# Kernel optimization log

Hardware: AMD Instinct MI355X
Metric: run time of the kernel (lower is better)

The kernel has to match this reference:

```python
import jax, jax.numpy as jnp
import numpy as np

L, N, E, H = 1024, 8, 1024, 8


def setup_inputs() -> dict:
    key = jax.random.key(0)
    ks = jax.random.split(key, 9)
    s = 0.02
    return {
        "query": jax.random.normal(ks[0], (L, N, E), jnp.float32),
        "key": jax.random.normal(ks[1], (L, N, E), jnp.float32),
        "value": jax.random.normal(ks[2], (L, N, E), jnp.float32),
        "Wqkv": jax.random.normal(ks[3], (H, 3 * E, E), jnp.float32) * s,
        "bqkv": jax.random.normal(ks[4], (H, 3 * E), jnp.float32) * s,
        "Wo": jax.random.normal(ks[5], (H, E, E), jnp.float32) * s,
        "bo": jax.random.normal(ks[6], (H, E), jnp.float32) * s,
        "Wout": jax.random.normal(ks[7], (E, H * E), jnp.float32) * s,
        "bout": jax.random.normal(ks[8], (E,), jnp.float32) * s,
    }


def reference(query, key, value, Wqkv, bqkv, Wo, bo, Wout, bout):
    # Each of H independent single-head MultiheadAttention modules, batched over h.
    Wq, Wk, Wv = Wqkv[:, :E], Wqkv[:, E:2 * E], Wqkv[:, 2 * E:]   # [H,E,E] each
    bq, bk, bv = bqkv[:, :E], bqkv[:, E:2 * E], bqkv[:, 2 * E:]   # [H,E]
    # Projections: (L,N,E) x (H,E,E) -> (H,L,N,E)
    q = jnp.einsum('lne,hde->hlnd', query, Wq) + bq[:, None, None, :]
    k = jnp.einsum('sne,hde->hsnd', key, Wk) + bk[:, None, None, :]
    v = jnp.einsum('sne,hde->hsnd', value, Wv) + bv[:, None, None, :]
    scale = 1.0 / jnp.sqrt(jnp.asarray(E, q.dtype))  # head_dim == E since 1 head per module
    scores = jnp.einsum('hlnd,hsnd->hnls', q, k) * scale  # [H,N,L,S]
    attn_weights = jax.nn.softmax(scores, axis=-1)
    ctx = jnp.einsum('hnls,hsnd->hlnd', attn_weights, v)   # [H,L,N,E]
    head_out = jnp.einsum('hlnd,hed->hlne', ctx, Wo) + bo[:, None, None, :]
    # concat along last dim: (L,N,H*E)
    concat = jnp.transpose(head_out, (1, 2, 0, 3)).reshape(L, N, H * E)
    out = concat @ Wout.T + bout  # (L,N,E)
    return out, attn_weights  # weights: [H,N,L,S] (stack of per-head (N,L,S))
```

## Files before the change

kernel.cpp:

```cpp
#include <hip/hip_runtime.h>
#include <stdint.h>


typedef unsigned short u16;
typedef unsigned int u32;
typedef __attribute__((ext_vector_type(8))) __bf16 bf16x8;
typedef __attribute__((ext_vector_type(4))) float f32x4;
typedef __attribute__((ext_vector_type(4))) u16 u16x4;

#define DEVFN static __device__ __forceinline__

static constexpr int LQ = 1024, NN = 8, EE = 1024, HH = 8, SS = 1024;
static constexpr long LNE = (long)LQ * NN * EE;
static constexpr long MM = 1048576;

static constexpr long OF_QBF   = 0;
static constexpr long OF_KBF   = 8388608;
static constexpr long OF_VALT  = 16777216;
static constexpr long OF_F     = 25165824;
static constexpr long OF_WKT   = 33554432;
static constexpr long OF_WVT   = 41943040;
static constexpr long OF_WOT   = 50331648;
static constexpr long OF_WOUTB = 58720256;
static constexpr long OF_GT    = 67108864;
static constexpr long OF_BM    = 75497472;
static constexpr long OF_T     = 83886080;
static constexpr long OF_P     = 150994944;
static constexpr long OF_SMALL_F = 109051904;

DEVFN u16 f2bf(float x) {
  u32 u = __builtin_bit_cast(u32, x);
  u = (u + 0x7FFFu + ((u >> 16) & 1u)) >> 16;
  return (u16)u;
}
DEVFN float bf2f(u16 x) { return __builtin_bit_cast(float, (u32)x << 16); }

DEVFN void gload16(const u16* g, u16* l) {
  __builtin_amdgcn_global_load_lds(
      (const __attribute__((address_space(1))) void*)(uintptr_t)g,
      (__attribute__((address_space(3))) void*)(uintptr_t)l, 16, 0, 0);
}

#define BAR() asm volatile("s_barrier" ::: "memory")
#define VMCNT2() asm volatile("s_waitcnt vmcnt(2)" ::: "memory")
#define VMCNT0() asm volatile("s_waitcnt vmcnt(0)" ::: "memory")
#define VMCNT8() asm volatile("s_waitcnt vmcnt(8)" ::: "memory")
#define VMCNT9() asm volatile("s_waitcnt vmcnt(9)" ::: "memory")
#define SB0() __builtin_amdgcn_sched_barrier(0)

struct Cvt3P { const float* s[3]; u16* d[3]; };
__global__ __launch_bounds__(256) void k_cvt3(Cvt3P p) {
  const int z = blockIdx.y;
  const float* s = p.s[z];
  u16* d = p.d[z];
  long i = (long)blockIdx.x * 256 + threadIdx.x;
  for (; i < 2097152; i += 131072) {
    float4 v = reinterpret_cast<const float4*>(s)[i];
    u16x4 o;
    o.x = f2bf(v.x); o.y = f2bf(v.y); o.z = f2bf(v.z); o.w = f2bf(v.w);
    reinterpret_cast<u16x4*>(d)[i] = o;
  }
}

struct Tp5P { const float* s[5]; u16* d[5]; int sld[5]; long szs[5]; long dzs[5]; };
__global__ __launch_bounds__(256) void k_tp5(Tp5P p) {
  const int cfg = blockIdx.z >> 3, zz = blockIdx.z & 7;
  const float* src = p.s[cfg] + (long)zz * p.szs[cfg];
  u16* dst = p.d[cfg] + (long)zz * p.dzs[cfg];
  const int sld = p.sld[cfg];
  __shared__ float t[64][65];
  const int r = threadIdx.x >> 4, c4 = (threadIdx.x & 15) * 4;
#pragma unroll
  for (int rr = 0; rr < 64; rr += 16) {
    float4 v = *reinterpret_cast<const float4*>(
        &src[(long)(blockIdx.y * 64 + r + rr) * sld + blockIdx.x * 64 + c4]);
    t[r + rr][c4] = v.x; t[r + rr][c4 + 1] = v.y;
    t[r + rr][c4 + 2] = v.z; t[r + rr][c4 + 3] = v.w;
  }
  __syncthreads();
#pragma unroll
  for (int rr = 0; rr < 64; rr += 16) {
    u16x4 o;
    o.x = f2bf(t[c4][r + rr]);     o.y = f2bf(t[c4 + 1][r + rr]);
    o.z = f2bf(t[c4 + 2][r + rr]); o.w = f2bf(t[c4 + 3][r + rr]);
    *reinterpret_cast<u16x4*>(
        &dst[(long)(blockIdx.x * 64 + r + rr) * 1024 + blockIdx.y * 64 + c4]) = o;
  }
}

__global__ __launch_bounds__(256) void k_bvec(const float* __restrict__ Wqkv,
                                              const float* __restrict__ bqkv,
                                              float* __restrict__ bp) {
  const int ec = blockIdx.x, h = blockIdx.y, dc = blockIdx.z, t = threadIdx.x;
  const int e = ec * 256 + t;
  const float* wk = Wqkv + (long)h * 3145728 + 1048576;
  const float* bq = bqkv + h * 3072;
  float sb = 0.f;
  for (int dd = 0; dd < 128; ++dd) {
    const int d = dc * 128 + dd;
    sb += wk[(long)d * 1024 + e] * bq[d];
  }
  bp[dc * 8192 + h * 1024 + e] = sb;
}
__global__ __launch_bounds__(256) void k_redb(const float* __restrict__ bp,
                                              float* __restrict__ b) {
  const int i = blockIdx.x * 256 + threadIdx.x;
  float sb = 0.f;
#pragma unroll
  for (int dc = 0; dc < 8; ++dc) sb += bp[dc * 8192 + i];
  b[i] = sb;
}

__global__ __launch_bounds__(256) void k_rowdot(const float* __restrict__ X,
                                                const float* __restrict__ V,
                                                float* __restrict__ OUT) {
  const int wave = threadIdx.x >> 6, lane = threadIdx.x & 63;
  const int r = blockIdx.x * 4 + wave;
  const float4* xr = reinterpret_cast<const float4*>(X + (long)r * 1024);
  float acc[8];
#pragma unroll
  for (int h = 0; h < 8; ++h) acc[h] = 0.f;
#pragma unroll
  for (int it = 0; it < 4; ++it) {
    float4 q = xr[it * 64 + lane];
#pragma unroll
    for (int h = 0; h < 8; ++h) {
      float4 av = reinterpret_cast<const float4*>(V + h * 1024)[it * 64 + lane];
      acc[h] += q.x * av.x + q.y * av.y + q.z * av.z + q.w * av.w;
    }
  }
#pragma unroll
  for (int h = 0; h < 8; ++h)
#pragma unroll
    for (int o = 1; o < 64; o <<= 1) acc[h] += __shfl_xor(acc[h], o);
  if (lane == 0) {
    const int idx = r >> 3, n = r & 7;
#pragma unroll
    for (int h = 0; h < 8; ++h) OUT[h * 8192 + n * 1024 + idx] = acc[h];
  }
}

__global__ __launch_bounds__(256) void k_be2(const float* __restrict__ Wout,
                                             const float* __restrict__ bo,
                                             const float* __restrict__ bout,
                                             const float* __restrict__ bqkv,
                                             const u16* __restrict__ Bm,
                                             float* __restrict__ be2) {
  const int e = blockIdx.x, t = threadIdx.x;
  float s = 0.f;
  for (int i = t; i < 8192; i += 256) {
    s += Wout[(long)e * 8192 + i] * bo[i];
    const int h = i >> 10, d = i & 1023;
    s += bf2f(Bm[(long)e * 8192 + i]) * bqkv[h * 3072 + 2048 + d];
  }
#pragma unroll
  for (int o = 1; o < 64; o <<= 1) s += __shfl_xor(s, o);
  __shared__ float ps[4];
  if ((t & 63) == 0) ps[t >> 6] = s;
  __syncthreads();
  if (t == 0) be2[e] = bout[e] + ps[0] + ps[1] + ps[2] + ps[3];
}

__global__ __launch_bounds__(256) void k_combine4(const float* __restrict__ pt,
                                                  const float* __restrict__ be,
                                                  float* __restrict__ out) {
  long i = (long)blockIdx.x * 256 + threadIdx.x;
  const long st = (long)gridDim.x * 256;
  for (; i < 2097152; i += st) {
    float4 a = reinterpret_cast<const float4*>(pt)[i];
    float4 b = reinterpret_cast<const float4*>(pt + 8388608)[i];
    float4 cc = reinterpret_cast<const float4*>(pt + 16777216)[i];
    float4 d = reinterpret_cast<const float4*>(pt + 25165824)[i];
    float4 e = reinterpret_cast<const float4*>(be)[i & 255];
    float4 o = {a.x + b.x + cc.x + d.x + e.x, a.y + b.y + cc.y + d.y + e.y,
                a.z + b.z + cc.z + d.z + e.z, a.w + b.w + cc.w + d.w + e.w};
    reinterpret_cast<float4*>(out)[i] = o;
  }
}

struct GemmP {
  const u16* A; const u16* B;
  float* Cf; u16* Cb;
  int lda, ldb, ldc, K, NB;
  long sAh, sAn, sBh, sBn, sCh, sCn;
  float scale;
};
struct GemmP2 { GemmP p0, p1; int split; };

template <int M0, int N0>
DEVFN void quad(f32x4 (&acc)[8][4], bf16x8 (&a)[4][2], bf16x8 (&b)[4][2]) {
#pragma unroll
  for (int mi = 0; mi < 4; ++mi)
#pragma unroll
    for (int ni = 0; ni < 2; ++ni) {
      acc[M0 + mi][N0 + ni] = __builtin_amdgcn_mfma_f32_16x16x32_bf16(
          a[mi][0], b[N0 + ni][0], acc[M0 + mi][N0 + ni], 0, 0, 0);
      acc[M0 + mi][N0 + ni] = __builtin_amdgcn_mfma_f32_16x16x32_bf16(
          a[mi][1], b[N0 + ni][1], acc[M0 + mi][N0 + ni], 0, 0, 0);
    }
}

DEVFN void swz_block(int& bx, int& by, int& bz) {
  long lid = blockIdx.x + (long)gridDim.x * (blockIdx.y + (long)gridDim.y * blockIdx.z);
  const long nwg = (long)gridDim.x * gridDim.y * gridDim.z;
  long s = (nwg % 8 == 0) ? ((lid % 8) * (nwg / 8) + lid / 8) : lid;
  bx = (int)(s % gridDim.x);
  long r2 = s / gridDim.x;
  by = (int)(r2 % gridDim.y);
  bz = (int)(r2 / gridDim.y);
}

template <int OUT_F32>
DEVFN void gemm_body(const GemmP& p, int bx, int by, int bz) {
  const int h = bz / p.NB, n = bz % p.NB;
  const u16* Ab = p.A + (long)h * p.sAh + (long)n * p.sAn;
  const u16* Bb = p.B + (long)h * p.sBh + (long)n * p.sBn;
  const long coff = (long)h * p.sCh + (long)n * p.sCn;
  const int row0 = by * 256;
  const int col0 = bx * 256;

  __shared__ u16 LDSU[65536];

  const int tid = threadIdx.x;
  const int wave = tid >> 6, lane = tid & 63;
  const int wr = wave >> 2, wc = wave & 3;
  const int NT = p.K >> 6;

  f32x4 acc[8][4];
  const f32x4 zero = {0.f, 0.f, 0.f, 0.f};
#pragma unroll
  for (int i = 0; i < 8; ++i)
#pragma unroll
    for (int j = 0; j < 4; ++j) acc[i][j] = zero;

  const int swc = ((lane & 7) ^ ((lane >> 3) & 7)) * 8;
  const u16* Ag = Ab + (long)(row0 + wave * 16 + (lane >> 3)) * p.lda + swc;
  const u16* Bg = Bb + (long)(col0 + wave * 16 + (lane >> 3)) * p.ldb + swc;

  auto STAGE = [&](int hh) {
    const int kt = hh >> 2;
    if (kt < NT) {
      const int pt = hh & 3;
      const int hf = pt >> 1;
      u16* l = &LDSU[((pt & 1) ? 32768 : 0) + (kt & 1) * 16384 + hf * 8192 + wave * 1024];
      const int ld = (pt & 1) ? p.ldb : p.lda;
      const u16* g = ((pt & 1) ? Bg : Ag) + (long)hf * 128 * ld + kt * 64;
      gload16(g, l);
      gload16(g + 8L * ld, l + 512);
    }
  };

  STAGE(0); STAGE(1); STAGE(2); STAGE(3); STAGE(4);
  VMCNT2();
  BAR();

  const int rA = lane & 15;
  const int c0 = (((lane >> 4)) ^ (lane & 7)) * 8;
  const int c1 = ((4 + (lane >> 4)) ^ (lane & 7)) * 8;

  bf16x8 a[4][2], b[4][2];

  for (int t = 0; t < NT; ++t) {
    const int db = (t & 1) * 16384;
    const u16* Ar = &LDSU[db + wr * 8192 + rA * 64];
    const u16* Br = &LDSU[32768 + db + (wc >> 1) * 8192 + ((wc & 1) * 64 + rA) * 64];

#pragma unroll
    for (int mi = 0; mi < 4; ++mi) {
      a[mi][0] = *reinterpret_cast<const bf16x8*>(&Ar[mi * 1024 + c0]);
      a[mi][1] = *reinterpret_cast<const bf16x8*>(&Ar[mi * 1024 + c1]);
    }
#pragma unroll
    for (int ni = 0; ni < 2; ++ni) {
      b[ni][0] = *reinterpret_cast<const bf16x8*>(&Br[ni * 1024 + c0]);
      b[ni][1] = *reinterpret_cast<const bf16x8*>(&Br[ni * 1024 + c1]);
    }
    STAGE(4 * t + 5);
    BAR();
    SB0(); __builtin_amdgcn_s_setprio(1);
    quad<0, 0>(acc, a, b);
    __builtin_amdgcn_s_setprio(0); SB0();
    BAR();

#pragma unroll
    for (int ni = 2; ni < 4; ++ni) {
      b[ni][0] = *reinterpret_cast<const bf16x8*>(&Br[ni * 1024 + c0]);
      b[ni][1] = *reinterpret_cast<const bf16x8*>(&Br[ni * 1024 + c1]);
    }
    STAGE(4 * t + 6);
    BAR();
    SB0(); __builtin_amdgcn_s_setprio(1);
    quad<0, 2>(acc, a, b);
    __builtin_amdgcn_s_setprio(0); SB0();
    BAR();

#pragma unroll
    for (int mi = 0; mi < 4; ++mi) {
      a[mi][0] = *reinterpret_cast<const bf16x8*>(&Ar[(4 + mi) * 1024 + c0]);
      a[mi][1] = *reinterpret_cast<const bf16x8*>(&Ar[(4 + mi) * 1024 + c1]);
    }
    STAGE(4 * t + 7);
    BAR();
    SB0(); __builtin_amdgcn_s_setprio(1);
    quad<4, 0>(acc, a, b);
    __builtin_amdgcn_s_setprio(0); SB0();
    BAR();

    STAGE(4 * t + 8);
    if (t < NT - 2) { VMCNT2(); }
    else if (t == NT - 2) { VMCNT0(); }
    BAR();
    SB0(); __builtin_amdgcn_s_setprio(1);
    quad<4, 2>(acc, a, b);
    __builtin_amdgcn_s_setprio(0); SB0();
    BAR();
  }

  const int crow = (lane >> 4) * 4;
  const int ccol = lane & 15;
#pragma unroll
  for (int mi = 0; mi < 8; ++mi) {
#pragma unroll
    for (int j = 0; j < 4; ++j) {
      const int grow = row0 + wr * 128 + mi * 16 + crow + j;
#pragma unroll
      for (int ni = 0; ni < 4; ++ni) {
        const int gcol = col0 + wc * 64 + ni * 16 + ccol;
        float v = acc[mi][ni][j] * p.scale;
        if constexpr (OUT_F32)
          p.Cf[coff + (long)grow * p.ldc + gcol] = v;
        else
          p.Cb[coff + (long)grow * p.ldc + gcol] = f2bf(v);
      }
    }
  }
}

template <int OUT_F32>
__global__ __launch_bounds__(512, 2) void k_gemm256(GemmP p) {
  int bx, by, bz;
  swz_block(bx, by, bz);
  gemm_body<OUT_F32>(p, bx, by, bz);
}
template <int OUT_F32>
__global__ __launch_bounds__(512, 2) void k_gemm256_pair(GemmP2 pp) {
  int bx, by, bz;
  swz_block(bx, by, bz);
  if (bz < pp.split) gemm_body<OUT_F32>(pp.p0, bx, by, bz);
  else gemm_body<OUT_F32>(pp.p1, bx, by, bz - pp.split);
}

struct FscP {
  const u16* T; const u16* K; const float* beta;
  float* attn; u16* P;
};
__global__ __launch_bounds__(512, 2) void k_fsc(FscP p) {
  int bx, by, bz;
  swz_block(bx, by, bz);
  const int h = by >> 3, n = by & 7;
  const int row0 = bx * 64;

  __shared__ u16 Abuf[2][64][64];
  __shared__ u16 Bbuf[2][8][128][32];
  __shared__ float red[2][64][8];

  const int tid = threadIdx.x;
  const int w = tid >> 6, lane = tid & 63;
  const int rl = lane & 15, g = lane >> 4;

  const u16* Abase = p.T + (long)h * 8388608 + n * 1024 + (long)row0 * 8192;
  const u16* Bbase = p.K + n * 1024;
  const float* betap = p.beta + h * 8192 + n * 1024 + w * 128 + rl;

  float betv[8];
#pragma unroll
  for (int ni = 0; ni < 8; ++ni) betv[ni] = betap[ni * 16];

  f32x4 acc[4][8];
  const f32x4 zero = {0.f, 0.f, 0.f, 0.f};
#pragma unroll
  for (int mi = 0; mi < 4; ++mi)
#pragma unroll
    for (int ni = 0; ni < 8; ++ni) acc[mi][ni] = zero;

  const u16* Bg = Bbase + (long)(w * 128 + (lane >> 2)) * 8192 +
                  ((lane & 3) ^ ((lane >> 2) & 3)) * 8;
  const u16* Ag = Abase + (long)(w * 8 + (lane >> 3)) * 8192 +
                  ((lane & 7) ^ ((lane >> 3) & 7)) * 8;

  auto STAGE_B = [&](int j) {
    u16* l = &Bbuf[j & 1][w][0][0];
    const u16* gp = Bg + (long)j * 32;
#pragma unroll
    for (int i = 0; i < 8; ++i) gload16(gp + (long)i * 16 * 8192, l + i * 512);
  };
  auto STAGE_A = [&](int pp2) {
    gload16(Ag + (long)pp2 * 64, &Abuf[pp2 & 1][w * 8][0]);
  };

  STAGE_B(0); STAGE_A(0); STAGE_B(1); STAGE_A(1);

  const int cA0 = ((g) ^ (lane & 7)) * 8;
  const int cA1 = ((4 + g) ^ (lane & 7)) * 8;
  const int cB = (g ^ (lane & 3)) * 8;

  for (int t2 = 0; t2 < 16; ++t2) {
    const int pb = t2 & 1;
    VMCNT9();
    BAR();
    {
      bf16x8 aF[4], bF[8];
#pragma unroll
      for (int mi = 0; mi < 4; ++mi)
        aF[mi] = *reinterpret_cast<const bf16x8*>(&Abuf[pb][mi * 16 + rl][cA0]);
#pragma unroll
      for (int ni = 0; ni < 8; ++ni)
        bF[ni] = *reinterpret_cast<const bf16x8*>(&Bbuf[0][w][ni * 16 + rl][cB]);
      SB0(); __builtin_amdgcn_s_setprio(1);
#pragma unroll
      for (int mi = 0; mi < 4; ++mi)
#pragma unroll
        for (int ni = 0; ni < 8; ++ni)
          acc[mi][ni] = __builtin_amdgcn_mfma_f32_16x16x32_bf16(
              aF[mi], bF[ni], acc[mi][ni], 0, 0, 0);
      __builtin_amdgcn_s_setprio(0); SB0();
    }
    BAR();
    if (t2 < 15) STAGE_B(2 * t2 + 2);
    VMCNT8();
    BAR();
    {
      bf16x8 aF[4], bF[8];
#pragma unroll
      for (int mi = 0; mi < 4; ++mi)
        aF[mi] = *reinterpret_cast<const bf16x8*>(&Abuf[pb][mi * 16 + rl][cA1]);
#pragma unroll
      for (int ni = 0; ni < 8; ++ni)
        bF[ni] = *reinterpret_cast<const bf16x8*>(&Bbuf[1][w][ni * 16 + rl][cB]);
      SB0(); __builtin_amdgcn_s_setprio(1);
#pragma unroll
      for (int mi = 0; mi < 4; ++mi)
#pragma unroll
        for (int ni = 0; ni < 8; ++ni)
          acc[mi][ni] = __builtin_amdgcn_mfma_f32_16x16x32_bf16(
              aF[mi], bF[ni], acc[mi][ni], 0, 0, 0);
      __builtin_amdgcn_s_setprio(0); SB0();
    }
    BAR();
    if (t2 < 15) STAGE_B(2 * t2 + 3);
    if (t2 < 14) STAGE_A(t2 + 2);
  }

  float rmax[4][4];
#pragma unroll
  for (int mi = 0; mi < 4; ++mi)
#pragma unroll
    for (int j = 0; j < 4; ++j) {
      float m = -3.0e38f;
#pragma unroll
      for (int ni = 0; ni < 8; ++ni) {
        float v = (acc[mi][ni][j] + betv[ni]) * 0.03125f;
        acc[mi][ni][j] = v;
        m = fmaxf(m, v);
      }
      rmax[mi][j] = m;
    }
#pragma unroll
  for (int msk = 1; msk < 16; msk <<= 1)
#pragma unroll
    for (int mi = 0; mi < 4; ++mi)
#pragma unroll
      for (int j = 0; j < 4; ++j)
        rmax[mi][j] = fmaxf(rmax[mi][j], __shfl_xor(rmax[mi][j], msk));
  if (rl == 0) {
#pragma unroll
    for (int mi = 0; mi < 4; ++mi)
#pragma unroll
      for (int j = 0; j < 4; ++j) red[0][mi * 16 + g * 4 + j][w] = rmax[mi][j];
  }
  __syncthreads();
  float gmax[4][4];
#pragma unroll
  for (int mi = 0; mi < 4; ++mi)
#pragma unroll
    for (int j = 0; j < 4; ++j) {
      const int row = mi * 16 + g * 4 + j;
      float4 x = *reinterpret_cast<const float4*>(&red[0][row][0]);
      float4 y = *reinterpret_cast<const float4*>(&red[0][row][4]);
      gmax[mi][j] = fmaxf(fmaxf(fmaxf(x.x, x.y), fmaxf(x.z, x.w)),
                          fmaxf(fmaxf(y.x, y.y), fmaxf(y.z, y.w)));
    }
  float rsum[4][4];
#pragma unroll
  for (int mi = 0; mi < 4; ++mi)
#pragma unroll
    for (int j = 0; j < 4; ++j) {
      float s = 0.f;
#pragma unroll
      for (int ni = 0; ni < 8; ++ni) {
        float e = __expf(acc[mi][ni][j] - gmax[mi][j]);
        acc[mi][ni][j] = e;
        s += e;
      }
      rsum[mi][j] = s;
    }
#pragma unroll
  for (int msk = 1; msk < 16; msk <<= 1)
#pragma unroll
    for (int mi = 0; mi < 4; ++mi)
#pragma unroll
      for (int j = 0; j < 4; ++j) rsum[mi][j] += __shfl_xor(rsum[mi][j], msk);
  if (rl == 0) {
#pragma unroll
    for (int mi = 0; mi < 4; ++mi)
#pragma unroll
      for (int j = 0; j < 4; ++j) red[1][mi * 16 + g * 4 + j][w] = rsum[mi][j];
  }
  __syncthreads();
  float* attn_b = p.attn + ((long)h * 8 + n) * 1048576;
  u16* P_b = p.P + ((long)h * 8 + n) * 1048576;
#pragma unroll
  for (int mi = 0; mi < 4; ++mi)
#pragma unroll
    for (int j = 0; j < 4; ++j) {
      const int row = mi * 16 + g * 4 + j;
      float4 x = *reinterpret_cast<const float4*>(&red[1][row][0]);
      float4 y = *reinterpret_cast<const float4*>(&red[1][row][4]);
      const float inv =
          1.0f / (x.x + x.y + x.z + x.w + y.x + y.y + y.z + y.w);
      float* ar = attn_b + (long)(row0 + row) * 1024 + w * 128 + rl;
      u16* pr = P_b + (long)(row0 + row) * 1024 + w * 128 + rl;
#pragma unroll
      for (int ni = 0; ni < 8; ++ni) {
        float v = acc[mi][ni][j] * inv;
        ar[ni * 16] = v;
        pr[ni * 16] = f2bf(v);
      }
    }
}

extern "C" void kernel_launch(void* const* d_in, const int* in_sizes, int n_in,
                              void* d_out, int out_size, void* d_ws,
                              size_t ws_size, hipStream_t stream) {
  const float* query = (const float*)d_in[0];
  const float* key_  = (const float*)d_in[1];
  const float* value = (const float*)d_in[2];
  const float* Wqkv  = (const float*)d_in[3];
  const float* bqkv  = (const float*)d_in[4];
  const float* Wo    = (const float*)d_in[5];
  const float* bo    = (const float*)d_in[6];
  const float* Wout  = (const float*)d_in[7];
  const float* bout  = (const float*)d_in[8];

  float* out  = (float*)d_out;
  float* attn = out + LNE;

  u16* ws = (u16*)d_ws;
  u16* qbf   = ws + OF_QBF;
  u16* kbf   = ws + OF_KBF;
  u16* valT  = ws + OF_VALT;
  u16* WqT_F = ws + OF_F;
  u16* WkT   = ws + OF_WKT;
  u16* WvT   = ws + OF_WVT;
  u16* WoT   = ws + OF_WOT;
  u16* Woutb = ws + OF_WOUTB;
  u16* Gt    = ws + OF_GT;
  u16* Bm    = ws + OF_BM;
  u16* Tbuf  = ws + OF_T;
  u16* Pbuf  = ws + OF_P;
  float* part = (float*)(ws + OF_P);
  float* Sf   = (float*)d_ws + OF_SMALL_F;
  float* beta  = Sf;
  float* bv2   = Sf + 65536;
  float* be2   = Sf + 73728;
  float* bpart = Sf + 74752;

  {
    Cvt3P p;
    p.s[0] = query; p.s[1] = key_; p.s[2] = Wout;
    p.d[0] = qbf;   p.d[1] = kbf;  p.d[2] = Woutb;
    k_cvt3<<<dim3(512, 3), 256, 0, stream>>>(p);
  }
  {
    Tp5P p;
    p.s[0] = Wqkv;           p.d[0] = WqT_F; p.sld[0] = 1024; p.szs[0] = 3145728; p.dzs[0] = MM;
    p.s[1] = Wqkv + 1048576; p.d[1] = WkT;   p.sld[1] = 1024; p.szs[1] = 3145728; p.dzs[1] = MM;
    p.s[2] = Wqkv + 2097152; p.d[2] = WvT;   p.sld[2] = 1024; p.szs[2] = 3145728; p.dzs[2] = MM;
    p.s[3] = Wo;             p.d[3] = WoT;   p.sld[3] = 1024; p.szs[3] = MM;      p.dzs[3] = MM;
    p.s[4] = value;          p.d[4] = valT;  p.sld[4] = 8192; p.szs[4] = 1024;    p.dzs[4] = MM;
    k_tp5<<<dim3(16, 16, 40), 256, 0, stream>>>(p);
  }
  k_bvec<<<dim3(4, 8, 8), 256, 0, stream>>>(Wqkv, bqkv, bpart);
  k_redb<<<32, 256, 0, stream>>>(bpart, bv2);
  k_rowdot<<<2048, 256, 0, stream>>>(key_, bv2, beta);

  const dim3 blk(512);

  {
    GemmP g = {};
    g.A = WkT; g.lda = 1024; g.sAh = MM; g.sAn = 0;
    g.B = WqT_F; g.ldb = 1024; g.sBh = MM; g.sBn = 0;
    g.Cb = Gt; g.ldc = 1024; g.sCh = MM; g.sCn = 0;
    g.K = 1024; g.NB = 1; g.scale = 1.f;
    GemmP m = {};
    m.A = Woutb; m.lda = 8192; m.sAh = 1024; m.sAn = 0;
    m.B = WoT; m.ldb = 1024; m.sBh = MM; m.sBn = 0;
    m.Cb = Bm; m.ldc = 8192; m.sCh = 1024; m.sCn = 0;
    m.K = 1024; m.NB = 1; m.scale = 1.f;
    GemmP2 pp = {g, m, 8};
    k_gemm256_pair<0><<<dim3(4, 4, 16), blk, 0, stream>>>(pp);
  }
  k_be2<<<1024, 256, 0, stream>>>(Wout, bo, bout, bqkv, Bm, be2);
  {
    GemmP t = {};
    t.A = qbf; t.lda = 8192; t.sAh = 0; t.sAn = 1024;
    t.B = Gt; t.ldb = 1024; t.sBh = MM; t.sBn = 0;
    t.Cb = Tbuf; t.ldc = 8192; t.sCh = 8388608; t.sCn = 1024;
    t.K = 1024; t.NB = 8; t.scale = 1.f;
    GemmP f = {};
    f.A = Bm; f.lda = 8192; f.sAh = 1024; f.sAn = 0;
    f.B = WvT; f.ldb = 1024; f.sBh = MM; f.sBn = 0;
    f.Cb = WqT_F; f.ldc = 8192; f.sCh = 1024; f.sCn = 0;
    f.K = 1024; f.NB = 1; f.scale = 1.f;
    GemmP2 pp = {t, f, 64};
    k_gemm256_pair<0><<<dim3(4, 4, 72), blk, 0, stream>>>(pp);
  }
  {
    FscP p = {Tbuf, kbf, beta, attn, Pbuf};
    k_fsc<<<dim3(16, 64), blk, 0, stream>>>(p);
  }
  {
    GemmP p = {};
    p.A = Pbuf; p.lda = 1024; p.sAh = 8388608; p.sAn = 1048576;
    p.B = valT; p.ldb = 1024; p.sBh = 0; p.sBn = 1048576;
    p.Cb = Tbuf; p.ldc = 65536; p.sCh = 1024; p.sCn = 8192;
    p.K = 1024; p.NB = 8; p.scale = 1.f;
    k_gemm256<0><<<dim3(4, 4, 64), blk, 0, stream>>>(p);
  }
  {
    GemmP p = {};
    p.A = Tbuf; p.lda = 8192; p.sAh = 2048; p.sAn = 0;
    p.B = WqT_F; p.ldb = 8192; p.sBh = 2048; p.sBn = 0;
    p.Cf = part; p.ldc = 1024; p.sCh = 8388608; p.sCn = 0;
    p.K = 2048; p.NB = 1; p.scale = 1.f;
    k_gemm256<1><<<dim3(4, 32, 4), blk, 0, stream>>>(p);
  }
  k_combine4<<<2048, 256, 0, stream>>>(part, be2, out);
}
```

Baseline: 991.6 us.

## Load K fragments directly into registers and ring-buffer A tiles in LDS

Reworks the k_fsc score kernel main loop so that the per-wave B (K) operand is loaded straight from global memory into registers, with double-buffered register prefetch, instead of being staged through LDS with global_load_lds. The A tile now goes global to register to LDS through a 4-deep ring buffer, with a single barrier per iteration instead of four. The intent is to cut LDS traffic and barrier and vmcnt stalls. In exchange it uses many more VGPRs for the B prefetch, which risks spills or lower occupancy at launch bounds (512,2), and the global B loads are less coalesced.

```diff
diff --git a/kernel.cpp b/kernel.cpp
--- a/kernel.cpp
+++ b/kernel.cpp
@@ -44,8 +44,7 @@
 #define BAR() asm volatile("s_barrier" ::: "memory")
 #define VMCNT2() asm volatile("s_waitcnt vmcnt(2)" ::: "memory")
 #define VMCNT0() asm volatile("s_waitcnt vmcnt(0)" ::: "memory")
-#define VMCNT8() asm volatile("s_waitcnt vmcnt(8)" ::: "memory")
-#define VMCNT9() asm volatile("s_waitcnt vmcnt(9)" ::: "memory")
+#define LGKM0() asm volatile("s_waitcnt lgkmcnt(0)" ::: "memory")
 #define SB0() __builtin_amdgcn_sched_barrier(0)
 
 struct Cvt3P { const float* s[3]; u16* d[3]; };
@@ -360,8 +359,7 @@
   const int h = by >> 3, n = by & 7;
   const int row0 = bx * 64;
 
-  __shared__ u16 Abuf[2][64][64];
-  __shared__ u16 Bbuf[2][8][128][32];
+  __shared__ u16 Abuf[4][64][64];
   __shared__ float red[2][64][8];
 
   const int tid = threadIdx.x;
@@ -369,12 +367,10 @@
   const int rl = lane & 15, g = lane >> 4;
 
   const u16* Abase = p.T + (long)h * 8388608 + n * 1024 + (long)row0 * 8192;
-  const u16* Bbase = p.K + n * 1024;
-  const float* betap = p.beta + h * 8192 + n * 1024 + w * 128 + rl;
-
-  float betv[8];
-#pragma unroll
-  for (int ni = 0; ni < 8; ++ni) betv[ni] = betap[ni * 16];
+  const u16* Ag = Abase + (long)(w * 8 + (lane >> 3)) * 8192 +
+                  ((lane & 7) ^ (lane >> 3)) * 8;
+  const int AwOff = (w * 8 + (lane >> 3)) * 64 + (lane & 7) * 8;
+  const u16* Bg = p.K + (long)(w * 128 + rl) * 8192 + n * 1024 + g * 8;
 
   f32x4 acc[4][8];
   const f32x4 zero = {0.f, 0.f, 0.f, 0.f};
@@ -383,73 +379,77 @@
 #pragma unroll
     for (int ni = 0; ni < 8; ++ni) acc[mi][ni] = zero;
 
-  const u16* Bg = Bbase + (long)(w * 128 + (lane >> 2)) * 8192 +
-                  ((lane & 3) ^ ((lane >> 2) & 3)) * 8;
-  const u16* Ag = Abase + (long)(w * 8 + (lane >> 3)) * 8192 +
-                  ((lane & 7) ^ ((lane >> 3) & 7)) * 8;
-
-  auto STAGE_B = [&](int j) {
-    u16* l = &Bbuf[j & 1][w][0][0];
-    const u16* gp = Bg + (long)j * 32;
-#pragma unroll
-    for (int i = 0; i < 8; ++i) gload16(gp + (long)i * 16 * 8192, l + i * 512);
-  };
-  auto STAGE_A = [&](int pp2) {
-    gload16(Ag + (long)pp2 * 64, &Abuf[pp2 & 1][w * 8][0]);
-  };
-
-  STAGE_B(0); STAGE_A(0); STAGE_B(1); STAGE_A(1);
-
-  const int cA0 = ((g) ^ (lane & 7)) * 8;
-  const int cA1 = ((4 + g) ^ (lane & 7)) * 8;
-  const int cB = (g ^ (lane & 3)) * 8;
-
-  for (int t2 = 0; t2 < 16; ++t2) {
-    const int pb = t2 & 1;
-    VMCNT9();
-    BAR();
-    {
-      bf16x8 aF[4], bF[8];
-#pragma unroll
-      for (int mi = 0; mi < 4; ++mi)
-        aF[mi] = *reinterpret_cast<const bf16x8*>(&Abuf[pb][mi * 16 + rl][cA0]);
+#pragma unroll
+  for (int P = 0; P < 4; ++P) {
+    bf16x8 ar = *reinterpret_cast<const bf16x8*>(Ag + P * 64);
+    *reinterpret_cast<bf16x8*>(&Abuf[0][0][0] + P * 4096 + AwOff) = ar;
+  }
+  bf16x8 bc[8], bn[8];
+#pragma unroll
+  for (int ni = 0; ni < 8; ++ni)
+    bc[ni] = *reinterpret_cast<const bf16x8*>(Bg + (long)ni * 131072);
+#pragma unroll
+  for (int ni = 0; ni < 8; ++ni)
+    bn[ni] = *reinterpret_cast<const bf16x8*>(Bg + (long)ni * 131072 + 32);
+  bf16x8 aregC = *reinterpret_cast<const bf16x8*>(Ag + 4 * 64);
+  bf16x8 aregN = aregC;
+  LGKM0();
+  BAR();
+
+  const int cA0 = (g ^ (rl & 7)) * 8;
+  const int cA1 = ((4 + g) ^ (rl & 7)) * 8;
+
+  for (int pq = 0; pq < 16; ++pq) {
+    const u16* Ab_ = &Abuf[pq & 3][0][0];
+    if (pq < 11)
+      aregN = *reinterpret_cast<const bf16x8*>(Ag + (long)(pq + 5) * 64);
+    bf16x8 aF[4];
+#pragma unroll
+    for (int mi = 0; mi < 4; ++mi)
+      aF[mi] = *reinterpret_cast<const bf16x8*>(&Ab_[(mi * 16 + rl) * 64 + cA0]);
+    SB0(); __builtin_amdgcn_s_setprio(1);
+#pragma unroll
+    for (int mi = 0; mi < 4; ++mi)
 #pragma unroll
       for (int ni = 0; ni < 8; ++ni)
-        bF[ni] = *reinterpret_cast<const bf16x8*>(&Bbuf[0][w][ni * 16 + rl][cB]);
-      SB0(); __builtin_amdgcn_s_setprio(1);
-#pragma unroll
-      for (int mi = 0; mi < 4; ++mi)
-#pragma unroll
-        for (int ni = 0; ni < 8; ++ni)
-          acc[mi][ni] = __builtin_amdgcn_mfma_f32_16x16x32_bf16(
-              aF[mi], bF[ni], acc[mi][ni], 0, 0, 0);
-      __builtin_amdgcn_s_setprio(0); SB0();
-    }
-    BAR();
-    if (t2 < 15) STAGE_B(2 * t2 + 2);
-    VMCNT8();
-    BAR();
-    {
-      bf16x8 aF[4], bF[8];
-#pragma unroll
-      for (int mi = 0; mi < 4; ++mi)
-        aF[mi] = *reinterpret_cast<const bf16x8*>(&Abuf[pb][mi * 16 + rl][cA1]);
+        acc[mi][ni] = __builtin_amdgcn_mfma_f32_16x16x32_bf16(
+            aF[mi], bc[ni], acc[mi][ni], 0, 0, 0);
+    __builtin_amdgcn_s_setprio(0); SB0();
+    if (pq < 15) {
 #pragma unroll
       for (int ni = 0; ni < 8; ++ni)
-        bF[ni] = *reinterpret_cast<const bf16x8*>(&Bbuf[1][w][ni * 16 + rl][cB]);
-      SB0(); __builtin_amdgcn_s_setprio(1);
-#pragma unroll
-      for (int mi = 0; mi < 4; ++mi)
-#pragma unroll
-        for (int ni = 0; ni < 8; ++ni)
-          acc[mi][ni] = __builtin_amdgcn_mfma_f32_16x16x32_bf16(
-              aF[mi], bF[ni], acc[mi][ni], 0, 0, 0);
-      __builtin_amdgcn_s_setprio(0); SB0();
-    }
-    BAR();
-    if (t2 < 15) STAGE_B(2 * t2 + 3);
-    if (t2 < 14) STAGE_A(t2 + 2);
-  }
+        bc[ni] = *reinterpret_cast<const bf16x8*>(
+            Bg + (long)ni * 131072 + (2 * pq + 2) * 32);
+    }
+#pragma unroll
+    for (int mi = 0; mi < 4; ++mi)
+      aF[mi] = *reinterpret_cast<const bf16x8*>(&Ab_[(mi * 16 + rl) * 64 + cA1]);
+    SB0(); __builtin_amdgcn_s_setprio(1);
+#pragma unroll
+    for (int mi = 0; mi < 4; ++mi)
+#pragma unroll
+      for (int ni = 0; ni < 8; ++ni)
+        acc[mi][ni] = __builtin_amdgcn_mfma_f32_16x16x32_bf16(
+            aF[mi], bn[ni], acc[mi][ni], 0, 0, 0);
+    __builtin_amdgcn_s_setprio(0); SB0();
+    if (pq < 15) {
+#pragma unroll
+      for (int ni = 0; ni < 8; ++ni)
+        bn[ni] = *reinterpret_cast<const bf16x8*>(
+            Bg + (long)ni * 131072 + (2 * pq + 3) * 32);
+    }
+    LGKM0();
+    BAR();
+    if (pq < 12) {
+      *reinterpret_cast<bf16x8*>(&Abuf[0][0][0] + (pq & 3) * 4096 + AwOff) = aregC;
+      aregC = aregN;
+    }
+  }
+
+  const float* betap = p.beta + h * 8192 + n * 1024 + w * 128 + rl;
+  float betv[8];
+#pragma unroll
+  for (int ni = 0; ni < 8; ++ni) betv[ni] = betap[ni * 16];
 
   float rmax[4][4];
 #pragma unroll
```

Measured after the change: 1.023 ms. +3.2%, slower.

## Restage fused score-softmax kernel pipeline and halve split-K partials in output GEMM

Applied to the files above, without the earlier changes.

The score+softmax kernel gets a new LDS layout: K tiles are staged as 32-wide k-slices in a large double-buffered BT array, and A goes into a 4-deep ring loaded by only half the waves. The loop becomes one MFMA phase per step with deeper prefetch and per-wave vmcnt waits. The final output projection splits K into 2 chunks instead of 4, so the combine kernel reads only two partial buffers. This trades less partial-buffer traffic for fewer blocks in the last GEMM, and a much larger LDS footprint in k_fsc that may lower occupancy.

```diff
diff --git a/kernel.cpp b/kernel.cpp
--- a/kernel.cpp
+++ b/kernel.cpp
@@ -45,7 +45,7 @@
 #define VMCNT2() asm volatile("s_waitcnt vmcnt(2)" ::: "memory")
 #define VMCNT0() asm volatile("s_waitcnt vmcnt(0)" ::: "memory")
 #define VMCNT8() asm volatile("s_waitcnt vmcnt(8)" ::: "memory")
-#define VMCNT9() asm volatile("s_waitcnt vmcnt(9)" ::: "memory")
+#define VMCNT10() asm volatile("s_waitcnt vmcnt(10)" ::: "memory")
 #define SB0() __builtin_amdgcn_sched_barrier(0)
 
 struct Cvt3P { const float* s[3]; u16* d[3]; };
@@ -161,19 +161,17 @@
   if (t == 0) be2[e] = bout[e] + ps[0] + ps[1] + ps[2] + ps[3];
 }
 
-__global__ __launch_bounds__(256) void k_combine4(const float* __restrict__ pt,
-                                                  const float* __restrict__ be,
-                                                  float* __restrict__ out) {
+__global__ __launch_bounds__(256) void k_combine(const float* __restrict__ p0,
+                                                 const float* __restrict__ p1,
+                                                 const float* __restrict__ be,
+                                                 float* __restrict__ out) {
   long i = (long)blockIdx.x * 256 + threadIdx.x;
   const long st = (long)gridDim.x * 256;
   for (; i < 2097152; i += st) {
-    float4 a = reinterpret_cast<const float4*>(pt)[i];
-    float4 b = reinterpret_cast<const float4*>(pt + 8388608)[i];
-    float4 cc = reinterpret_cast<const float4*>(pt + 16777216)[i];
-    float4 d = reinterpret_cast<const float4*>(pt + 25165824)[i];
-    float4 e = reinterpret_cast<const float4*>(be)[i & 255];
-    float4 o = {a.x + b.x + cc.x + d.x + e.x, a.y + b.y + cc.y + d.y + e.y,
-                a.z + b.z + cc.z + d.z + e.z, a.w + b.w + cc.w + d.w + e.w};
+    float4 a = reinterpret_cast<const float4*>(p0)[i];
+    float4 b = reinterpret_cast<const float4*>(p1)[i];
+    float4 c = reinterpret_cast<const float4*>(be)[i & 255];
+    float4 o = {a.x + b.x + c.x, a.y + b.y + c.y, a.z + b.z + c.z, a.w + b.w + c.w};
     reinterpret_cast<float4*>(out)[i] = o;
   }
 }
@@ -360,21 +358,17 @@
   const int h = by >> 3, n = by & 7;
   const int row0 = bx * 64;
 
-  __shared__ u16 Abuf[2][64][64];
-  __shared__ u16 Bbuf[2][8][128][32];
+  __shared__ u16 BT[65536];
+  __shared__ u16 AT[8192];
   __shared__ float red[2][64][8];
 
   const int tid = threadIdx.x;
   const int w = tid >> 6, lane = tid & 63;
-  const int rl = lane & 15, g = lane >> 4;
+  const int rl = lane & 15, g4 = lane >> 4;
 
   const u16* Abase = p.T + (long)h * 8388608 + n * 1024 + (long)row0 * 8192;
-  const u16* Bbase = p.K + n * 1024;
-  const float* betap = p.beta + h * 8192 + n * 1024 + w * 128 + rl;
-
-  float betv[8];
-#pragma unroll
-  for (int ni = 0; ni < 8; ++ni) betv[ni] = betap[ni * 16];
+  const u16* AsrcL = Abase + (long)lane * 8192;
+  const u16* BsrcL = p.K + n * 1024 + (long)lane * 8192;
 
   f32x4 acc[4][8];
   const f32x4 zero = {0.f, 0.f, 0.f, 0.f};
@@ -383,73 +377,59 @@
 #pragma unroll
     for (int ni = 0; ni < 8; ++ni) acc[mi][ni] = zero;
 
-  const u16* Bg = Bbase + (long)(w * 128 + (lane >> 2)) * 8192 +
-                  ((lane & 3) ^ ((lane >> 2) & 3)) * 8;
-  const u16* Ag = Abase + (long)(w * 8 + (lane >> 3)) * 8192 +
-                  ((lane & 7) ^ ((lane >> 3) & 7)) * 8;
-
-  auto STAGE_B = [&](int j) {
-    u16* l = &Bbuf[j & 1][w][0][0];
-    const u16* gp = Bg + (long)j * 32;
-#pragma unroll
-    for (int i = 0; i < 8; ++i) gload16(gp + (long)i * 16 * 8192, l + i * 512);
+  auto STAGE_B = [&](int t) {
+    const int bufo = (t & 1) * 32768;
+#pragma unroll
+    for (int q8 = 0; q8 < 8; ++q8) {
+      const int q = w * 8 + q8;
+      const int g = q >> 4, cb = q & 15;
+      gload16(BsrcL + (long)cb * 524288 + t * 32 + g * 8,
+              &BT[bufo + g * 8192 + cb * 512]);
+    }
   };
-  auto STAGE_A = [&](int pp2) {
-    gload16(Ag + (long)pp2 * 64, &Abuf[pp2 & 1][w * 8][0]);
+  auto STAGE_A = [&](int t) {
+    gload16(AsrcL + t * 32 + w * 8, &AT[(t & 3) * 2048 + w * 512]);
   };
 
-  STAGE_B(0); STAGE_A(0); STAGE_B(1); STAGE_A(1);
-
-  const int cA0 = ((g) ^ (lane & 7)) * 8;
-  const int cA1 = ((4 + g) ^ (lane & 7)) * 8;
-  const int cB = (g ^ (lane & 3)) * 8;
-
-  for (int t2 = 0; t2 < 16; ++t2) {
-    const int pb = t2 & 1;
-    VMCNT9();
-    BAR();
-    {
-      bf16x8 aF[4], bF[8];
-#pragma unroll
-      for (int mi = 0; mi < 4; ++mi)
-        aF[mi] = *reinterpret_cast<const bf16x8*>(&Abuf[pb][mi * 16 + rl][cA0]);
+  STAGE_B(0); STAGE_B(1);
+  if (w < 4) { STAGE_A(0); STAGE_A(1); STAGE_A(2); }
+  if (w < 4) { VMCNT10(); } else { VMCNT8(); }
+  BAR();
+
+  const int NT = 32;
+  for (int t = 0; t < NT; ++t) {
+    const u16* Ab_ = &AT[(t & 3) * 2048 + g4 * 512];
+    const u16* Bb_ = &BT[(t & 1) * 32768 + g4 * 8192];
+    bf16x8 aF[4], bF[8];
+#pragma unroll
+    for (int mi = 0; mi < 4; ++mi)
+      aF[mi] = *reinterpret_cast<const bf16x8*>(&Ab_[(mi * 16 + rl) * 8]);
+#pragma unroll
+    for (int ni = 0; ni < 8; ++ni)
+      bF[ni] = *reinterpret_cast<const bf16x8*>(&Bb_[(w * 128 + ni * 16 + rl) * 8]);
+    SB0(); __builtin_amdgcn_s_setprio(1);
+#pragma unroll
+    for (int mi = 0; mi < 4; ++mi)
 #pragma unroll
       for (int ni = 0; ni < 8; ++ni)
-        bF[ni] = *reinterpret_cast<const bf16x8*>(&Bbuf[0][w][ni * 16 + rl][cB]);
-      SB0(); __builtin_amdgcn_s_setprio(1);
-#pragma unroll
-      for (int mi = 0; mi < 4; ++mi)
-#pragma unroll
-        for (int ni = 0; ni < 8; ++ni)
-          acc[mi][ni] = __builtin_amdgcn_mfma_f32_16x16x32_bf16(
-              aF[mi], bF[ni], acc[mi][ni], 0, 0, 0);
-      __builtin_amdgcn_s_setprio(0); SB0();
-    }
-    BAR();
-    if (t2 < 15) STAGE_B(2 * t2 + 2);
-    VMCNT8();
-    BAR();
-    {
-      bf16x8 aF[4], bF[8];
-#pragma unroll
-      for (int mi = 0; mi < 4; ++mi)
-        aF[mi] = *reinterpret_cast<const bf16x8*>(&Abuf[pb][mi * 16 + rl][cA1]);
-#pragma unroll
-      for (int ni = 0; ni < 8; ++ni)
-        bF[ni] = *reinterpret_cast<const bf16x8*>(&Bbuf[1][w][ni * 16 + rl][cB]);
-      SB0(); __builtin_amdgcn_s_setprio(1);
-#pragma unroll
-      for (int mi = 0; mi < 4; ++mi)
-#pragma unroll
-        for (int ni = 0; ni < 8; ++ni)
-          acc[mi][ni] = __builtin_amdgcn_mfma_f32_16x16x32_bf16(
-              aF[mi], bF[ni], acc[mi][ni], 0, 0, 0);
-      __builtin_amdgcn_s_setprio(0); SB0();
-    }
-    BAR();
-    if (t2 < 15) STAGE_B(2 * t2 + 3);
-    if (t2 < 14) STAGE_A(t2 + 2);
-  }
+        acc[mi][ni] = __builtin_amdgcn_mfma_f32_16x16x32_bf16(
+            aF[mi], bF[ni], acc[mi][ni], 0, 0, 0);
+    __builtin_amdgcn_s_setprio(0); SB0();
+    BAR();
+    if (t + 2 < NT) STAGE_B(t + 2);
+    if (w < 4 && t + 3 < NT) STAGE_A(t + 3);
+    if (t < NT - 2) {
+      if (w < 4) { VMCNT10(); } else { VMCNT8(); }
+    } else {
+      VMCNT0();
+    }
+    BAR();
+  }
+
+  const float* betap = p.beta + h * 8192 + n * 1024 + w * 128 + rl;
+  float betv[8];
+#pragma unroll
+  for (int ni = 0; ni < 8; ++ni) betv[ni] = betap[ni * 16];
 
   float rmax[4][4];
 #pragma unroll
@@ -476,7 +456,7 @@
 #pragma unroll
     for (int mi = 0; mi < 4; ++mi)
 #pragma unroll
-      for (int j = 0; j < 4; ++j) red[0][mi * 16 + g * 4 + j][w] = rmax[mi][j];
+      for (int j = 0; j < 4; ++j) red[0][mi * 16 + g4 * 4 + j][w] = rmax[mi][j];
   }
   __syncthreads();
   float gmax[4][4];
@@ -484,7 +464,7 @@
   for (int mi = 0; mi < 4; ++mi)
 #pragma unroll
     for (int j = 0; j < 4; ++j) {
-      const int row = mi * 16 + g * 4 + j;
+      const int row = mi * 16 + g4 * 4 + j;
       float4 x = *reinterpret_cast<const float4*>(&red[0][row][0]);
       float4 y = *reinterpret_cast<const float4*>(&red[0][row][4]);
       gmax[mi][j] = fmaxf(fmaxf(fmaxf(x.x, x.y), fmaxf(x.z, x.w)),
@@ -514,7 +494,7 @@
 #pragma unroll
     for (int mi = 0; mi < 4; ++mi)
 #pragma unroll
-      for (int j = 0; j < 4; ++j) red[1][mi * 16 + g * 4 + j][w] = rsum[mi][j];
+      for (int j = 0; j < 4; ++j) red[1][mi * 16 + g4 * 4 + j][w] = rsum[mi][j];
   }
   __syncthreads();
   float* attn_b = p.attn + ((long)h * 8 + n) * 1048576;
@@ -523,7 +503,7 @@
   for (int mi = 0; mi < 4; ++mi)
 #pragma unroll
     for (int j = 0; j < 4; ++j) {
-      const int row = mi * 16 + g * 4 + j;
+      const int row = mi * 16 + g4 * 4 + j;
       float4 x = *reinterpret_cast<const float4*>(&red[1][row][0]);
       float4 y = *reinterpret_cast<const float4*>(&red[1][row][4]);
       const float inv =
@@ -639,11 +619,11 @@
   }
   {
     GemmP p = {};
-    p.A = Tbuf; p.lda = 8192; p.sAh = 2048; p.sAn = 0;
-    p.B = WqT_F; p.ldb = 8192; p.sBh = 2048; p.sBn = 0;
+    p.A = Tbuf; p.lda = 8192; p.sAh = 4096; p.sAn = 0;
+    p.B = WqT_F; p.ldb = 8192; p.sBh = 4096; p.sBn = 0;
     p.Cf = part; p.ldc = 1024; p.sCh = 8388608; p.sCn = 0;
-    p.K = 2048; p.NB = 1; p.scale = 1.f;
-    k_gemm256<1><<<dim3(4, 32, 4), blk, 0, stream>>>(p);
-  }
-  k_combine4<<<2048, 256, 0, stream>>>(part, be2, out);
-}
+    p.K = 4096; p.NB = 1; p.scale = 1.f;
+    k_gemm256<1><<<dim3(4, 32, 2), blk, 0, stream>>>(p);
+  }
+  k_combine<<<2048, 256, 0, stream>>>(part, part + 8388608, be2, out);
+}
```

Result: slower. 1.130 ms (+13.9%).
